# Kernel optimization log

Hardware: AMD Instinct MI355X
Metric: run time of the kernel (lower is better)

Reference implementation:

```python
import jax, jax.numpy as jnp
import numpy as np

B, S, HID, H, DK = 2, 2048, 1024, 16, 64
SCALE = DK ** -0.5
NEG = -1000000000.0


def setup_inputs() -> dict:
    key = jax.random.key(0)
    ks = jax.random.split(key, 14)
    std = HID ** -0.5
    return {
        "q": jax.random.normal(ks[0], (B, S, HID), jnp.float32),
        "k": jax.random.normal(ks[1], (B, S, HID), jnp.float32),
        "v": jax.random.normal(ks[2], (B, S, HID), jnp.float32),
        "attn_bias": jax.random.normal(ks[3], (B, H, S, S), jnp.float32),
        "mask": jax.random.randint(ks[4], (B, S), 0, 2, jnp.int32),
        "Wq": jax.random.normal(ks[5], (HID, H * DK), jnp.float32) * std,
        "bq": jnp.zeros((H * DK,), jnp.float32),
        "Wk": jax.random.normal(ks[6], (HID, H * DK), jnp.float32) * std,
        "bk": jnp.zeros((H * DK,), jnp.float32),
        "Wv": jax.random.normal(ks[7], (HID, H * DK), jnp.float32) * std,
        "bv": jnp.zeros((H * DK,), jnp.float32),
        "Wo": jax.random.normal(ks[8], (H * DK, H * DK), jnp.float32) * std,
        "bo": jnp.zeros((H * DK,), jnp.float32),
    }


def reference(q, k, v, attn_bias, mask, Wq, bq, Wk, bk, Wv, bv, Wo, bo):
    Bq = q.shape[0]
    # projections -> [B, H, S, DK]
    qh = (q @ Wq + bq).reshape(Bq, -1, H, DK).transpose(0, 2, 1, 3) * SCALE
    kh = (k @ Wk + bk).reshape(Bq, -1, H, DK).transpose(0, 2, 1, 3)
    vh = (v @ Wv + bv).reshape(Bq, -1, H, DK).transpose(0, 2, 1, 3)
    # scores [B, H, Sq, Sk]
    scores = jnp.einsum("bhqd,bhkd->bhqk", qh, kh)
    k_mask = mask[:, None, None, :]  # [B,1,1,Sk]
    scores = jnp.where(k_mask == 0, NEG, scores)
    scores = scores + attn_bias
    attn = jax.nn.softmax(scores, axis=-1)  # dropout rate 0.0 -> identity
    x = jnp.einsum("bhqk,bhkd->bhqd", attn, vh)
    x = x * mask[:, None, :, None].astype(x.dtype)  # zero masked query rows
    x = x.transpose(0, 2, 1, 3).reshape(Bq, -1, H * DK)
    return x @ Wo + bo
```

## Files before the change

### kernel.cpp

```cpp
#include <hip/hip_runtime.h>


typedef __bf16 bf16x8 __attribute__((ext_vector_type(8)));
typedef float f32x4 __attribute__((ext_vector_type(4)));
typedef unsigned short u16x8 __attribute__((ext_vector_type(8)));

#define NEGV (-1000000000.0f)

static __device__ __forceinline__ unsigned short f2b(float f) {
  unsigned int u = __float_as_uint(f);
  unsigned int r = (u + 0x7FFFu + ((u >> 16) & 1u)) >> 16;
  return (unsigned short)r;
}

static __device__ __forceinline__ bf16x8 lds_ld8(const unsigned short* p) {
  return __builtin_bit_cast(bf16x8, *(const u16x8*)p);
}

__global__ __launch_bounds__(256) void k_wtrans(const float* __restrict__ W,
                                                unsigned short* __restrict__ Wt) {
  __shared__ float tile[32][33];
  int k0 = blockIdx.x * 32, n0 = blockIdx.y * 32;
  int tx = threadIdx.x, ty = threadIdx.y;
  #pragma unroll
  for (int i = 0; i < 32; i += 8)
    tile[ty + i][tx] = W[(size_t)(k0 + ty + i) * 1024 + n0 + tx];
  __syncthreads();
  #pragma unroll
  for (int i = 0; i < 32; i += 8)
    Wt[(size_t)(n0 + ty + i) * 1024 + k0 + tx] = f2b(tile[tx][ty + i]);
}

__global__ __launch_bounds__(256) void k_gemm(const float* __restrict__ Af,
                                              const unsigned short* __restrict__ Ab,
                                              const unsigned short* __restrict__ Bt,
                                              const float* __restrict__ bias,
                                              unsigned short* __restrict__ outb,
                                              float* __restrict__ outf, int mode) {
  __shared__ __align__(16) unsigned short As[64 * 72];
  __shared__ __align__(16) unsigned short Bs[64 * 72];
  int t = threadIdx.x;
  int wave = t >> 6, lane = t & 63;
  int r16 = lane & 15, quad = lane >> 4, quad8 = quad * 8;
  int w16 = wave * 16;
  int n0 = blockIdx.x * 64, m0 = blockIdx.y * 64;
  f32x4 acc[4] = {{0.f, 0.f, 0.f, 0.f}, {0.f, 0.f, 0.f, 0.f},
                  {0.f, 0.f, 0.f, 0.f}, {0.f, 0.f, 0.f, 0.f}};

  for (int k0 = 0; k0 < 1024; k0 += 64) {
    __syncthreads();
    if (mode != 3) {
      int tr = t >> 4, tc = (t & 15) * 4;
      #pragma unroll
      for (int i = 0; i < 64; i += 16) {
        const float* p = Af + (size_t)(m0 + tr + i) * 1024 + k0 + tc;
        float4 f = *(const float4*)p;
        ushort4 h;
        h.x = f2b(f.x); h.y = f2b(f.y); h.z = f2b(f.z); h.w = f2b(f.w);
        *(ushort4*)&As[(tr + i) * 72 + tc] = h;
      }
    } else {
      int tr = t >> 3, tc = (t & 7) * 8;
      #pragma unroll
      for (int i = 0; i < 64; i += 32) {
        int4 d = *(const int4*)(Ab + (size_t)(m0 + tr + i) * 1024 + k0 + tc);
        *(int4*)&As[(tr + i) * 72 + tc] = d;
      }
    }
    {
      int tr = t >> 3, tc = (t & 7) * 8;
      #pragma unroll
      for (int i = 0; i < 64; i += 32) {
        int4 d = *(const int4*)(Bt + (size_t)(n0 + tr + i) * 1024 + k0 + tc);
        *(int4*)&Bs[(tr + i) * 72 + tc] = d;
      }
    }
    __syncthreads();
    #pragma unroll
    for (int kk = 0; kk < 64; kk += 32) {
      bf16x8 a = lds_ld8(&As[(w16 + r16) * 72 + kk + quad8]);
      #pragma unroll
      for (int nt = 0; nt < 4; nt++) {
        bf16x8 bb = lds_ld8(&Bs[(nt * 16 + r16) * 72 + kk + quad8]);
        acc[nt] = __builtin_amdgcn_mfma_f32_16x16x32_bf16(a, bb, acc[nt], 0, 0, 0);
      }
    }
  }

  if (mode == 2) {
    __syncthreads();
    #pragma unroll
    for (int nt = 0; nt < 4; nt++) {
      float bv = bias[n0 + nt * 16 + r16];
      #pragma unroll
      for (int r = 0; r < 4; r++)
        As[(nt * 16 + r16) * 72 + (w16 + quad * 4 + r)] = f2b(acc[nt][r] + bv);
    }
    __syncthreads();
    int bidx = m0 >> 11, s0 = m0 & 2047, h = n0 >> 6;
    int nl = t >> 2, mc = (t & 3) * 16;
    size_t o = ((size_t)(bidx * 16 + h) * 64 + nl) * 2048 + s0 + mc;
    int4 d0 = *(const int4*)&As[nl * 72 + mc];
    int4 d1 = *(const int4*)&As[nl * 72 + mc + 8];
    *(int4*)(outb + o) = d0;
    *(int4*)(outb + o + 8) = d1;
  } else if (mode == 3) {
    #pragma unroll
    for (int nt = 0; nt < 4; nt++) {
      int gn = n0 + nt * 16 + r16;
      float bv = bias[gn];
      #pragma unroll
      for (int r = 0; r < 4; r++) {
        int gm = m0 + w16 + quad * 4 + r;
        outf[(size_t)gm * 1024 + gn] = acc[nt][r] + bv;
      }
    }
  } else {
    float scale = (mode == 0) ? 0.125f : 1.0f;
    #pragma unroll
    for (int nt = 0; nt < 4; nt++) {
      int gn = n0 + nt * 16 + r16;
      float bv = bias[gn];
      int h = gn >> 6, d = gn & 63;
      #pragma unroll
      for (int r = 0; r < 4; r++) {
        int gm = m0 + w16 + quad * 4 + r;
        int bidx = gm >> 11, s = gm & 2047;
        outb[((size_t)(bidx * 16 + h) * 2048 + s) * 64 + d] =
            f2b((acc[nt][r] + bv) * scale);
      }
    }
  }
}

__global__ __launch_bounds__(256) void k_attn(const unsigned short* __restrict__ qh,
                                              const unsigned short* __restrict__ kh,
                                              const unsigned short* __restrict__ vt,
                                              const float* __restrict__ bias,
                                              const int* __restrict__ mask,
                                              unsigned short* __restrict__ xb) {
  __shared__ __align__(16) unsigned short Qs[64 * 72];
  __shared__ __align__(16) unsigned short Ks[64 * 72];
  __shared__ __align__(16) unsigned short Vs[64 * 72];
  __shared__ __align__(16) unsigned short Ps[64 * 72];
  __shared__ float kmb[64];
  int t = threadIdx.x;
  int wave = t >> 6, lane = t & 63;
  int r16 = lane & 15, quad = lane >> 4, quad8 = quad * 8;
  int w16 = wave * 16;
  int q0 = blockIdx.x * 64;
  int bh = blockIdx.y;
  int b = bh >> 4, h = bh & 15;
  const unsigned short* qbase = qh + (size_t)bh * 2048 * 64;
  const unsigned short* kbase = kh + (size_t)bh * 2048 * 64;
  const unsigned short* vbase = vt + (size_t)bh * 64 * 2048;
  const float* bbase = bias + (size_t)bh * 2048 * 2048 + (size_t)q0 * 2048;

  {
    int row = t >> 2, c = (t & 3) * 16;
    int4 d0 = *(const int4*)(qbase + (size_t)(q0 + row) * 64 + c);
    int4 d1 = *(const int4*)(qbase + (size_t)(q0 + row) * 64 + c + 8);
    *(int4*)&Qs[row * 72 + c] = d0;
    *(int4*)&Qs[row * 72 + c + 8] = d1;
  }

  f32x4 o[4] = {{0.f, 0.f, 0.f, 0.f}, {0.f, 0.f, 0.f, 0.f},
                {0.f, 0.f, 0.f, 0.f}, {0.f, 0.f, 0.f, 0.f}};
  float mrow[4] = {-1e38f, -1e38f, -1e38f, -1e38f};
  float lrow[4] = {0.f, 0.f, 0.f, 0.f};

  for (int k0 = 0; k0 < 2048; k0 += 64) {
    __syncthreads();
    {
      int row = t >> 2, c = (t & 3) * 16;
      int4 a0 = *(const int4*)(kbase + (size_t)(k0 + row) * 64 + c);
      int4 a1 = *(const int4*)(kbase + (size_t)(k0 + row) * 64 + c + 8);
      *(int4*)&Ks[row * 72 + c] = a0;
      *(int4*)&Ks[row * 72 + c + 8] = a1;
      int4 b0 = *(const int4*)(vbase + (size_t)row * 2048 + k0 + c);
      int4 b1 = *(const int4*)(vbase + (size_t)row * 2048 + k0 + c + 8);
      *(int4*)&Vs[row * 72 + c] = b0;
      *(int4*)&Vs[row * 72 + c + 8] = b1;
    }
    if (t < 64) kmb[t] = (mask[b * 2048 + k0 + t] == 0) ? 1.0f : 0.0f;
    __syncthreads();

    f32x4 sc[4] = {{0.f, 0.f, 0.f, 0.f}, {0.f, 0.f, 0.f, 0.f},
                   {0.f, 0.f, 0.f, 0.f}, {0.f, 0.f, 0.f, 0.f}};
    #pragma unroll
    for (int kk = 0; kk < 64; kk += 32) {
      bf16x8 a = lds_ld8(&Qs[(w16 + r16) * 72 + kk + quad8]);
      #pragma unroll
      for (int nt = 0; nt < 4; nt++) {
        bf16x8 bb = lds_ld8(&Ks[(nt * 16 + r16) * 72 + kk + quad8]);
        sc[nt] = __builtin_amdgcn_mfma_f32_16x16x32_bf16(a, bb, sc[nt], 0, 0, 0);
      }
    }
    #pragma unroll
    for (int nt = 0; nt < 4; nt++) {
      float km = kmb[nt * 16 + r16];
      #pragma unroll
      for (int r = 0; r < 4; r++) {
        float bval = bbase[(size_t)(w16 + quad * 4 + r) * 2048 + k0 + nt * 16 + r16];
        float sv = (km > 0.5f) ? NEGV : sc[nt][r];
        sc[nt][r] = sv + bval;
      }
    }
    float arow[4];
    #pragma unroll
    for (int r = 0; r < 4; r++) {
      float mx = fmaxf(fmaxf(sc[0][r], sc[1][r]), fmaxf(sc[2][r], sc[3][r]));
      #pragma unroll
      for (int off = 1; off < 16; off <<= 1) mx = fmaxf(mx, __shfl_xor(mx, off));
      float mn = fmaxf(mrow[r], mx);
      float ps = 0.f;
      #pragma unroll
      for (int nt = 0; nt < 4; nt++) {
        float p = __expf(sc[nt][r] - mn);
        sc[nt][r] = p;
        ps += p;
      }
      #pragma unroll
      for (int off = 1; off < 16; off <<= 1) ps += __shfl_xor(ps, off);
      float al = __expf(mrow[r] - mn);
      lrow[r] = lrow[r] * al + ps;
      mrow[r] = mn;
      arow[r] = al;
    }
    #pragma unroll
    for (int nt = 0; nt < 4; nt++)
      #pragma unroll
      for (int r = 0; r < 4; r++)
        Ps[(w16 + quad * 4 + r) * 72 + nt * 16 + r16] = f2b(sc[nt][r]);
    #pragma unroll
    for (int nt = 0; nt < 4; nt++)
      #pragma unroll
      for (int r = 0; r < 4; r++) o[nt][r] *= arow[r];
    #pragma unroll
    for (int kk = 0; kk < 64; kk += 32) {
      bf16x8 a = lds_ld8(&Ps[(w16 + r16) * 72 + kk + quad8]);
      #pragma unroll
      for (int nt = 0; nt < 4; nt++) {
        bf16x8 bb = lds_ld8(&Vs[(nt * 16 + r16) * 72 + kk + quad8]);
        o[nt] = __builtin_amdgcn_mfma_f32_16x16x32_bf16(a, bb, o[nt], 0, 0, 0);
      }
    }
  }

  float inv[4], qm[4];
  #pragma unroll
  for (int r = 0; r < 4; r++) {
    int gq = q0 + w16 + quad * 4 + r;
    qm[r] = (mask[b * 2048 + gq] != 0) ? 1.0f : 0.0f;
    inv[r] = 1.0f / lrow[r];
  }
  #pragma unroll
  for (int nt = 0; nt < 4; nt++) {
    #pragma unroll
    for (int r = 0; r < 4; r++) {
      int gq = q0 + w16 + quad * 4 + r;
      float val = o[nt][r] * inv[r] * qm[r];
      xb[(size_t)(b * 2048 + gq) * 1024 + h * 64 + nt * 16 + r16] = f2b(val);
    }
  }
}

extern "C" void kernel_launch(void* const* d_in, const int* in_sizes, int n_in,
                              void* d_out, int out_size, void* d_ws, size_t ws_size,
                              hipStream_t stream) {
  const float* q = (const float*)d_in[0];
  const float* k = (const float*)d_in[1];
  const float* v = (const float*)d_in[2];
  const float* attn_bias = (const float*)d_in[3];
  const int* mask = (const int*)d_in[4];
  const float* Wq = (const float*)d_in[5];
  const float* bq = (const float*)d_in[6];
  const float* Wk = (const float*)d_in[7];
  const float* bk = (const float*)d_in[8];
  const float* Wv = (const float*)d_in[9];
  const float* bv = (const float*)d_in[10];
  const float* Wo = (const float*)d_in[11];
  const float* bo = (const float*)d_in[12];

  char* ws = (char*)d_ws;
  const size_t MB = 1u << 20;
  unsigned short* Wqt = (unsigned short*)(ws + 0 * MB);
  unsigned short* Wkt = (unsigned short*)(ws + 2 * MB);
  unsigned short* Wvt = (unsigned short*)(ws + 4 * MB);
  unsigned short* Wot = (unsigned short*)(ws + 6 * MB);
  unsigned short* qhb = (unsigned short*)(ws + 8 * MB);
  unsigned short* khb = (unsigned short*)(ws + 16 * MB);
  unsigned short* vtb = (unsigned short*)(ws + 24 * MB);
  unsigned short* xbb = (unsigned short*)(ws + 32 * MB);

  dim3 tg(32, 32), tb(32, 8);
  k_wtrans<<<tg, tb, 0, stream>>>(Wq, Wqt);
  k_wtrans<<<tg, tb, 0, stream>>>(Wk, Wkt);
  k_wtrans<<<tg, tb, 0, stream>>>(Wv, Wvt);
  k_wtrans<<<tg, tb, 0, stream>>>(Wo, Wot);

  dim3 gg(16, 64), gb(256);
  k_gemm<<<gg, gb, 0, stream>>>(q, nullptr, Wqt, bq, qhb, nullptr, 0);
  k_gemm<<<gg, gb, 0, stream>>>(k, nullptr, Wkt, bk, khb, nullptr, 1);
  k_gemm<<<gg, gb, 0, stream>>>(v, nullptr, Wvt, bv, vtb, nullptr, 2);

  k_attn<<<dim3(32, 32), 256, 0, stream>>>(qhb, khb, vtb, attn_bias, mask, xbb);

  k_gemm<<<gg, gb, 0, stream>>>(nullptr, xbb, Wot, bo, nullptr, (float*)d_out, 3);
}
```

Measured before the change: 900.1 us.

## Enlarge GEMM tiles with async LDS loads and swizzle; keep Q in registers

The projection GEMM moves to 128x128 block tiles with a 64x64 per-wave register tile. B, and A in the bf16 mode, are loaded with global_load_lds into an XOR-swizzled LDS layout, and outputs are staged through LDS for coalesced stores. The attention kernel keeps Q fragments in registers and computes the softmax row sum with an MFMA against a ones vector instead of shuffle reductions, and the four weight transposes are merged into one launch. The larger tiles use more registers and LDS and leave fewer blocks to fill the GPU.

```diff
diff --git a/kernel.cpp b/kernel.cpp
--- a/kernel.cpp
+++ b/kernel.cpp
@@ -7,18 +7,28 @@
 
 #define NEGV (-1000000000.0f)
 
+typedef __attribute__((address_space(3))) unsigned int lds_u32;
+typedef const __attribute__((address_space(1))) unsigned int glb_u32;
+
+static __device__ __forceinline__ void async16(const void* g, void* l) {
+  __builtin_amdgcn_global_load_lds((glb_u32*)g, (lds_u32*)l, 16, 0, 0);
+}
+
 static __device__ __forceinline__ unsigned short f2b(float f) {
   unsigned int u = __float_as_uint(f);
-  unsigned int r = (u + 0x7FFFu + ((u >> 16) & 1u)) >> 16;
-  return (unsigned short)r;
-}
-
-static __device__ __forceinline__ bf16x8 lds_ld8(const unsigned short* p) {
+  return (unsigned short)((u + 0x7FFFu + ((u >> 16) & 1u)) >> 16);
+}
+
+static __device__ __forceinline__ bf16x8 ld8(const unsigned short* p) {
   return __builtin_bit_cast(bf16x8, *(const u16x8*)p);
 }
 
-__global__ __launch_bounds__(256) void k_wtrans(const float* __restrict__ W,
-                                                unsigned short* __restrict__ Wt) {
+__global__ __launch_bounds__(256) void k_wtrans(const float* __restrict__ W0, const float* __restrict__ W1,
+                                                const float* __restrict__ W2, const float* __restrict__ W3,
+                                                unsigned short* __restrict__ T0, unsigned short* __restrict__ T1,
+                                                unsigned short* __restrict__ T2, unsigned short* __restrict__ T3) {
+  const float* W = (blockIdx.z == 0) ? W0 : (blockIdx.z == 1) ? W1 : (blockIdx.z == 2) ? W2 : W3;
+  unsigned short* Wt = (blockIdx.z == 0) ? T0 : (blockIdx.z == 1) ? T1 : (blockIdx.z == 2) ? T2 : T3;
   __shared__ float tile[32][33];
   int k0 = blockIdx.x * 32, n0 = blockIdx.y * 32;
   int tx = threadIdx.x, ty = threadIdx.y;
@@ -37,99 +47,115 @@
                                               const float* __restrict__ bias,
                                               unsigned short* __restrict__ outb,
                                               float* __restrict__ outf, int mode) {
-  __shared__ __align__(16) unsigned short As[64 * 72];
-  __shared__ __align__(16) unsigned short Bs[64 * 72];
+  __shared__ __align__(16) unsigned short smem[128 * 136];
+  unsigned short* As = smem;
+  unsigned short* Bs = smem + 128 * 64;
   int t = threadIdx.x;
   int wave = t >> 6, lane = t & 63;
   int r16 = lane & 15, quad = lane >> 4, quad8 = quad * 8;
-  int w16 = wave * 16;
-  int n0 = blockIdx.x * 64, m0 = blockIdx.y * 64;
-  f32x4 acc[4] = {{0.f, 0.f, 0.f, 0.f}, {0.f, 0.f, 0.f, 0.f},
-                  {0.f, 0.f, 0.f, 0.f}, {0.f, 0.f, 0.f, 0.f}};
+  int wm = (wave >> 1) * 64, wn = (wave & 1) * 64;
+  int n0 = blockIdx.x * 128, m0 = blockIdx.y * 128;
+  f32x4 acc[4][4] = {};
 
   for (int k0 = 0; k0 < 1024; k0 += 64) {
     __syncthreads();
     if (mode != 3) {
-      int tr = t >> 4, tc = (t & 15) * 4;
-      #pragma unroll
-      for (int i = 0; i < 64; i += 16) {
-        const float* p = Af + (size_t)(m0 + tr + i) * 1024 + k0 + tc;
-        float4 f = *(const float4*)p;
-        ushort4 h;
-        h.x = f2b(f.x); h.y = f2b(f.y); h.z = f2b(f.z); h.w = f2b(f.w);
-        *(ushort4*)&As[(tr + i) * 72 + tc] = h;
+      int g = t & 7;
+      #pragma unroll
+      for (int rr = 0; rr < 4; rr++) {
+        int row = (t >> 3) + rr * 32;
+        const float* p = Af + (size_t)(m0 + row) * 1024 + k0 + g * 8;
+        float4 f0 = *(const float4*)p;
+        float4 f1 = *(const float4*)(p + 4);
+        u16x8 h;
+        h[0] = f2b(f0.x); h[1] = f2b(f0.y); h[2] = f2b(f0.z); h[3] = f2b(f0.w);
+        h[4] = f2b(f1.x); h[5] = f2b(f1.y); h[6] = f2b(f1.z); h[7] = f2b(f1.w);
+        *(u16x8*)&As[row * 64 + ((g ^ (row & 7))) * 8] = h;
       }
     } else {
-      int tr = t >> 3, tc = (t & 7) * 8;
-      #pragma unroll
-      for (int i = 0; i < 64; i += 32) {
-        int4 d = *(const int4*)(Ab + (size_t)(m0 + tr + i) * 1024 + k0 + tc);
-        *(int4*)&As[(tr + i) * 72 + tc] = d;
-      }
-    }
-    {
-      int tr = t >> 3, tc = (t & 7) * 8;
-      #pragma unroll
-      for (int i = 0; i < 64; i += 32) {
-        int4 d = *(const int4*)(Bt + (size_t)(n0 + tr + i) * 1024 + k0 + tc);
-        *(int4*)&Bs[(tr + i) * 72 + tc] = d;
-      }
+      #pragma unroll
+      for (int i = 0; i < 4; i++) {
+        int row = wave * 32 + i * 8 + (lane >> 3);
+        const unsigned short* g = Ab + (size_t)(m0 + row) * 1024 + k0 + (((lane & 7) ^ (row & 7))) * 8;
+        async16(g, &As[(wave * 32 + i * 8) * 64]);
+      }
+    }
+    #pragma unroll
+    for (int i = 0; i < 4; i++) {
+      int row = wave * 32 + i * 8 + (lane >> 3);
+      const unsigned short* g = Bt + (size_t)(n0 + row) * 1024 + k0 + (((lane & 7) ^ (row & 7))) * 8;
+      async16(g, &Bs[(wave * 32 + i * 8) * 64]);
     }
     __syncthreads();
     #pragma unroll
-    for (int kk = 0; kk < 64; kk += 32) {
-      bf16x8 a = lds_ld8(&As[(w16 + r16) * 72 + kk + quad8]);
+    for (int kk2 = 0; kk2 < 2; kk2++) {
+      bf16x8 av[4], bv[4];
+      int gq = quad + kk2 * 4;
+      #pragma unroll
+      for (int mt = 0; mt < 4; mt++) {
+        int lm = wm + mt * 16 + r16;
+        av[mt] = ld8(&As[lm * 64 + (gq ^ (lm & 7)) * 8]);
+      }
       #pragma unroll
       for (int nt = 0; nt < 4; nt++) {
-        bf16x8 bb = lds_ld8(&Bs[(nt * 16 + r16) * 72 + kk + quad8]);
-        acc[nt] = __builtin_amdgcn_mfma_f32_16x16x32_bf16(a, bb, acc[nt], 0, 0, 0);
-      }
-    }
-  }
-
+        int ln = wn + nt * 16 + r16;
+        bv[nt] = ld8(&Bs[ln * 64 + (gq ^ (ln & 7)) * 8]);
+      }
+      #pragma unroll
+      for (int mt = 0; mt < 4; mt++)
+        #pragma unroll
+        for (int nt = 0; nt < 4; nt++)
+          acc[mt][nt] = __builtin_amdgcn_mfma_f32_16x16x32_bf16(av[mt], bv[nt], acc[mt][nt], 0, 0, 0);
+    }
+  }
+
+  if (mode == 3) {
+    #pragma unroll
+    for (int nt = 0; nt < 4; nt++) {
+      int gn = n0 + wn + nt * 16 + r16;
+      float bv = bias[gn];
+      #pragma unroll
+      for (int mt = 0; mt < 4; mt++)
+        #pragma unroll
+        for (int r = 0; r < 4; r++) {
+          int gm = m0 + wm + mt * 16 + quad * 4 + r;
+          outf[(size_t)gm * 1024 + gn] = acc[mt][nt][r] + bv;
+        }
+    }
+    return;
+  }
+
+  __syncthreads();
+  float scale = (mode == 0) ? 0.125f : 1.0f;
+  #pragma unroll
+  for (int nt = 0; nt < 4; nt++) {
+    int ln = wn + nt * 16 + r16;
+    float bv = bias[n0 + ln];
+    #pragma unroll
+    for (int mt = 0; mt < 4; mt++)
+      #pragma unroll
+      for (int r = 0; r < 4; r++) {
+        int lm = wm + mt * 16 + quad * 4 + r;
+        unsigned short hv = f2b((acc[mt][nt][r] + bv) * scale);
+        if (mode == 2) smem[ln * 136 + lm] = hv;
+        else           smem[lm * 136 + ln] = hv;
+      }
+  }
+  __syncthreads();
+  int rrow = t >> 1, half = t & 1;
+  const unsigned short* src = smem + rrow * 136 + half * 64;
   if (mode == 2) {
-    __syncthreads();
-    #pragma unroll
-    for (int nt = 0; nt < 4; nt++) {
-      float bv = bias[n0 + nt * 16 + r16];
-      #pragma unroll
-      for (int r = 0; r < 4; r++)
-        As[(nt * 16 + r16) * 72 + (w16 + quad * 4 + r)] = f2b(acc[nt][r] + bv);
-    }
-    __syncthreads();
-    int bidx = m0 >> 11, s0 = m0 & 2047, h = n0 >> 6;
-    int nl = t >> 2, mc = (t & 3) * 16;
-    size_t o = ((size_t)(bidx * 16 + h) * 64 + nl) * 2048 + s0 + mc;
-    int4 d0 = *(const int4*)&As[nl * 72 + mc];
-    int4 d1 = *(const int4*)&As[nl * 72 + mc + 8];
-    *(int4*)(outb + o) = d0;
-    *(int4*)(outb + o + 8) = d1;
-  } else if (mode == 3) {
-    #pragma unroll
-    for (int nt = 0; nt < 4; nt++) {
-      int gn = n0 + nt * 16 + r16;
-      float bv = bias[gn];
-      #pragma unroll
-      for (int r = 0; r < 4; r++) {
-        int gm = m0 + w16 + quad * 4 + r;
-        outf[(size_t)gm * 1024 + gn] = acc[nt][r] + bv;
-      }
-    }
+    int b = m0 >> 11, s0 = m0 & 2047;
+    int gn = n0 + rrow, h = gn >> 6, d = gn & 63;
+    unsigned short* dst = outb + ((size_t)(b * 16 + h) * 64 + d) * 2048 + s0 + half * 64;
+    #pragma unroll
+    for (int j = 0; j < 8; j++) *(int4*)(dst + j * 8) = *(const int4*)(src + j * 8);
   } else {
-    float scale = (mode == 0) ? 0.125f : 1.0f;
-    #pragma unroll
-    for (int nt = 0; nt < 4; nt++) {
-      int gn = n0 + nt * 16 + r16;
-      float bv = bias[gn];
-      int h = gn >> 6, d = gn & 63;
-      #pragma unroll
-      for (int r = 0; r < 4; r++) {
-        int gm = m0 + w16 + quad * 4 + r;
-        int bidx = gm >> 11, s = gm & 2047;
-        outb[((size_t)(bidx * 16 + h) * 2048 + s) * 64 + d] =
-            f2b((acc[nt][r] + bv) * scale);
-      }
-    }
+    int gm = m0 + rrow, b = gm >> 11, s = gm & 2047;
+    int h = (n0 + half * 64) >> 6;
+    unsigned short* dst = outb + ((size_t)(b * 16 + h) * 2048 + s) * 64;
+    #pragma unroll
+    for (int j = 0; j < 8; j++) *(int4*)(dst + j * 8) = *(const int4*)(src + j * 8);
   }
 }
 
@@ -139,7 +165,6 @@
                                               const float* __restrict__ bias,
                                               const int* __restrict__ mask,
                                               unsigned short* __restrict__ xb) {
-  __shared__ __align__(16) unsigned short Qs[64 * 72];
   __shared__ __align__(16) unsigned short Ks[64 * 72];
   __shared__ __align__(16) unsigned short Vs[64 * 72];
   __shared__ __align__(16) unsigned short Ps[64 * 72];
@@ -151,49 +176,42 @@
   int q0 = blockIdx.x * 64;
   int bh = blockIdx.y;
   int b = bh >> 4, h = bh & 15;
-  const unsigned short* qbase = qh + (size_t)bh * 2048 * 64;
   const unsigned short* kbase = kh + (size_t)bh * 2048 * 64;
   const unsigned short* vbase = vt + (size_t)bh * 64 * 2048;
   const float* bbase = bias + (size_t)bh * 2048 * 2048 + (size_t)q0 * 2048;
 
+  bf16x8 qf[2];
   {
-    int row = t >> 2, c = (t & 3) * 16;
-    int4 d0 = *(const int4*)(qbase + (size_t)(q0 + row) * 64 + c);
-    int4 d1 = *(const int4*)(qbase + (size_t)(q0 + row) * 64 + c + 8);
-    *(int4*)&Qs[row * 72 + c] = d0;
-    *(int4*)&Qs[row * 72 + c + 8] = d1;
-  }
-
-  f32x4 o[4] = {{0.f, 0.f, 0.f, 0.f}, {0.f, 0.f, 0.f, 0.f},
-                {0.f, 0.f, 0.f, 0.f}, {0.f, 0.f, 0.f, 0.f}};
+    const unsigned short* qrow = qh + (size_t)bh * 2048 * 64 + (size_t)(q0 + w16 + r16) * 64;
+    qf[0] = ld8(qrow + quad8);
+    qf[1] = ld8(qrow + 32 + quad8);
+  }
+  const u16x8 onesu = {0x3F80, 0x3F80, 0x3F80, 0x3F80, 0x3F80, 0x3F80, 0x3F80, 0x3F80};
+  const bf16x8 ones = __builtin_bit_cast(bf16x8, onesu);
+
+  f32x4 o[4] = {};
+  f32x4 accl = {};
   float mrow[4] = {-1e38f, -1e38f, -1e38f, -1e38f};
-  float lrow[4] = {0.f, 0.f, 0.f, 0.f};
 
   for (int k0 = 0; k0 < 2048; k0 += 64) {
     __syncthreads();
     {
       int row = t >> 2, c = (t & 3) * 16;
-      int4 a0 = *(const int4*)(kbase + (size_t)(k0 + row) * 64 + c);
-      int4 a1 = *(const int4*)(kbase + (size_t)(k0 + row) * 64 + c + 8);
-      *(int4*)&Ks[row * 72 + c] = a0;
-      *(int4*)&Ks[row * 72 + c + 8] = a1;
-      int4 b0 = *(const int4*)(vbase + (size_t)row * 2048 + k0 + c);
-      int4 b1 = *(const int4*)(vbase + (size_t)row * 2048 + k0 + c + 8);
-      *(int4*)&Vs[row * 72 + c] = b0;
-      *(int4*)&Vs[row * 72 + c + 8] = b1;
+      *(int4*)&Ks[row * 72 + c]     = *(const int4*)(kbase + (size_t)(k0 + row) * 64 + c);
+      *(int4*)&Ks[row * 72 + c + 8] = *(const int4*)(kbase + (size_t)(k0 + row) * 64 + c + 8);
+      *(int4*)&Vs[row * 72 + c]     = *(const int4*)(vbase + (size_t)row * 2048 + k0 + c);
+      *(int4*)&Vs[row * 72 + c + 8] = *(const int4*)(vbase + (size_t)row * 2048 + k0 + c + 8);
     }
     if (t < 64) kmb[t] = (mask[b * 2048 + k0 + t] == 0) ? 1.0f : 0.0f;
     __syncthreads();
 
-    f32x4 sc[4] = {{0.f, 0.f, 0.f, 0.f}, {0.f, 0.f, 0.f, 0.f},
-                   {0.f, 0.f, 0.f, 0.f}, {0.f, 0.f, 0.f, 0.f}};
-    #pragma unroll
-    for (int kk = 0; kk < 64; kk += 32) {
-      bf16x8 a = lds_ld8(&Qs[(w16 + r16) * 72 + kk + quad8]);
+    f32x4 sc[4] = {};
+    #pragma unroll
+    for (int kk2 = 0; kk2 < 2; kk2++) {
       #pragma unroll
       for (int nt = 0; nt < 4; nt++) {
-        bf16x8 bb = lds_ld8(&Ks[(nt * 16 + r16) * 72 + kk + quad8]);
-        sc[nt] = __builtin_amdgcn_mfma_f32_16x16x32_bf16(a, bb, sc[nt], 0, 0, 0);
+        bf16x8 bb = ld8(&Ks[(nt * 16 + r16) * 72 + kk2 * 32 + quad8]);
+        sc[nt] = __builtin_amdgcn_mfma_f32_16x16x32_bf16(qf[kk2], bb, sc[nt], 0, 0, 0);
       }
     }
     #pragma unroll
@@ -202,8 +220,7 @@
       #pragma unroll
       for (int r = 0; r < 4; r++) {
         float bval = bbase[(size_t)(w16 + quad * 4 + r) * 2048 + k0 + nt * 16 + r16];
-        float sv = (km > 0.5f) ? NEGV : sc[nt][r];
-        sc[nt][r] = sv + bval;
+        sc[nt][r] = ((km > 0.5f) ? NEGV : sc[nt][r]) + bval;
       }
     }
     float arow[4];
@@ -213,19 +230,10 @@
       #pragma unroll
       for (int off = 1; off < 16; off <<= 1) mx = fmaxf(mx, __shfl_xor(mx, off));
       float mn = fmaxf(mrow[r], mx);
-      float ps = 0.f;
-      #pragma unroll
-      for (int nt = 0; nt < 4; nt++) {
-        float p = __expf(sc[nt][r] - mn);
-        sc[nt][r] = p;
-        ps += p;
-      }
-      #pragma unroll
-      for (int off = 1; off < 16; off <<= 1) ps += __shfl_xor(ps, off);
-      float al = __expf(mrow[r] - mn);
-      lrow[r] = lrow[r] * al + ps;
+      arow[r] = __expf(mrow[r] - mn);
       mrow[r] = mn;
-      arow[r] = al;
+      #pragma unroll
+      for (int nt = 0; nt < 4; nt++) sc[nt][r] = __expf(sc[nt][r] - mn);
     }
     #pragma unroll
     for (int nt = 0; nt < 4; nt++)
@@ -233,36 +241,37 @@
       for (int r = 0; r < 4; r++)
         Ps[(w16 + quad * 4 + r) * 72 + nt * 16 + r16] = f2b(sc[nt][r]);
     #pragma unroll
-    for (int nt = 0; nt < 4; nt++)
-      #pragma unroll
-      for (int r = 0; r < 4; r++) o[nt][r] *= arow[r];
-    #pragma unroll
-    for (int kk = 0; kk < 64; kk += 32) {
-      bf16x8 a = lds_ld8(&Ps[(w16 + r16) * 72 + kk + quad8]);
+    for (int r = 0; r < 4; r++) {
+      accl[r] *= arow[r];
+      #pragma unroll
+      for (int nt = 0; nt < 4; nt++) o[nt][r] *= arow[r];
+    }
+    #pragma unroll
+    for (int kk2 = 0; kk2 < 2; kk2++) {
+      bf16x8 a = ld8(&Ps[(w16 + r16) * 72 + kk2 * 32 + quad8]);
+      accl = __builtin_amdgcn_mfma_f32_16x16x32_bf16(a, ones, accl, 0, 0, 0);
       #pragma unroll
       for (int nt = 0; nt < 4; nt++) {
-        bf16x8 bb = lds_ld8(&Vs[(nt * 16 + r16) * 72 + kk + quad8]);
+        bf16x8 bb = ld8(&Vs[(nt * 16 + r16) * 72 + kk2 * 32 + quad8]);
         o[nt] = __builtin_amdgcn_mfma_f32_16x16x32_bf16(a, bb, o[nt], 0, 0, 0);
       }
     }
   }
 
-  float inv[4], qm[4];
+  float inv[4];
   #pragma unroll
   for (int r = 0; r < 4; r++) {
     int gq = q0 + w16 + quad * 4 + r;
-    qm[r] = (mask[b * 2048 + gq] != 0) ? 1.0f : 0.0f;
-    inv[r] = 1.0f / lrow[r];
-  }
-  #pragma unroll
-  for (int nt = 0; nt < 4; nt++) {
+    float qm = (mask[b * 2048 + gq] != 0) ? 1.0f : 0.0f;
+    inv[r] = qm / accl[r];
+  }
+  #pragma unroll
+  for (int nt = 0; nt < 4; nt++)
     #pragma unroll
     for (int r = 0; r < 4; r++) {
       int gq = q0 + w16 + quad * 4 + r;
-      float val = o[nt][r] * inv[r] * qm[r];
-      xb[(size_t)(b * 2048 + gq) * 1024 + h * 64 + nt * 16 + r16] = f2b(val);
-    }
-  }
+      xb[(size_t)(b * 2048 + gq) * 1024 + h * 64 + nt * 16 + r16] = f2b(o[nt][r] * inv[r]);
+    }
 }
 
 extern "C" void kernel_launch(void* const* d_in, const int* in_sizes, int n_in,
@@ -293,13 +302,9 @@
   unsigned short* vtb = (unsigned short*)(ws + 24 * MB);
   unsigned short* xbb = (unsigned short*)(ws + 32 * MB);
 
-  dim3 tg(32, 32), tb(32, 8);
-  k_wtrans<<<tg, tb, 0, stream>>>(Wq, Wqt);
-  k_wtrans<<<tg, tb, 0, stream>>>(Wk, Wkt);
-  k_wtrans<<<tg, tb, 0, stream>>>(Wv, Wvt);
-  k_wtrans<<<tg, tb, 0, stream>>>(Wo, Wot);
-
-  dim3 gg(16, 64), gb(256);
+  k_wtrans<<<dim3(32, 32, 4), dim3(32, 8), 0, stream>>>(Wq, Wk, Wv, Wo, Wqt, Wkt, Wvt, Wot);
+
+  dim3 gg(8, 32), gb(256);
   k_gemm<<<gg, gb, 0, stream>>>(q, nullptr, Wqt, bq, qhb, nullptr, 0);
   k_gemm<<<gg, gb, 0, stream>>>(k, nullptr, Wkt, bk, khb, nullptr, 1);
   k_gemm<<<gg, gb, 0, stream>>>(v, nullptr, Wvt, bv, vtb, nullptr, 2);
```

New measurement: 927.9 us. 3.1% more time.
